# Kernel tuning notes

Measured on AMD Instinct MI355X. Metric: run time of the kernel, lower is better.

The kernel has to match this reference:

```python
import jax, jax.numpy as jnp
import numpy as np

BN_EPS = 1e-5


def setup_inputs() -> dict:
    key = jax.random.key(0)
    k1, k2 = jax.random.split(key, 2)
    b, C, h, w = 4, 256, 64, 64
    K = 16  # num_codes is hard-coded to 16 inside __init__
    x = jax.random.normal(k1, (b, C, h, w), dtype=jnp.float32)
    conv_w = jax.random.normal(k2, (K, C), dtype=jnp.float32) * (1.0 / np.sqrt(C))
    bn_gamma = jnp.ones((K,), dtype=jnp.float32)
    bn_beta = jnp.zeros((K,), dtype=jnp.float32)
    return {"x": x, "conv_w": conv_w, "bn_gamma": bn_gamma, "bn_beta": bn_beta}


def reference(x, conv_w, bn_gamma, bn_beta):
    b, C, h, w = x.shape
    K = conv_w.shape[0]
    hw = h * w

    # 1x1 conv (no bias) -> BatchNorm2d (training-mode batch stats) -> ReLU
    cw = jnp.einsum('kc,bchw->bkhw', conv_w, x)          # (b, K, h, w)
    mean = cw.mean(axis=(0, 2, 3))                        # (K,)
    var = cw.var(axis=(0, 2, 3))                          # biased variance, (K,)
    cw = (cw - mean[None, :, None, None]) * jax.lax.rsqrt(var + BN_EPS)[None, :, None, None]
    cw = cw * bn_gamma[None, :, None, None] + bn_beta[None, :, None, None]
    cw = jax.nn.relu(cw)

    cw_flat = cw.reshape(b, K, hw)                        # (b, K, hw)
    scale = cw_flat.mean(axis=2)                          # (b, K)
    # Faithful to torch: flat row-major reinterpretation of (b,K,hw) as (b,hw,K,1)
    r = cw_flat.reshape(b, hw, K, 1)                      # (b, hw, K, 1)

    x2 = x.reshape(b, C, hw).transpose(0, 2, 1)           # (b, hw, C)
    diff = x2[:, :, None, :] - r                          # (b, hw, K, C)

    scaled_l2 = scale[:, :, None] * jnp.sum(diff * diff, axis=1)   # (b, K, C)
    aw = jax.nn.softmax(scaled_l2, axis=1)                # softmax over K, (b, K, C)
    encoded_feat = jnp.sum(aw[:, None, :, :] * diff, axis=1)       # (b, K, C)
    return encoded_feat
```

## Files before the change

kernel.cpp:

```cpp
#include <hip/hip_runtime.h>

#define BN_EPS 1e-5f

#define OFF_PBN     0
#define OFF_PSR     16384
#define OFF_PSX     32768
#define OFF_PSXX    163840
#define OFF_CROSSR  294912
#define OFF_CW      360448
#define OFF_PCX     622592
#define WS_NEED     ((size_t)(OFF_PCX + 2097152) * sizeof(float))

#define FMA16(v, rp)                                     \
    {                                                    \
        const float4* rq_ = (const float4*)(rp);         \
        float4 r0_ = rq_[0], r1_ = rq_[1];               \
        float4 r2_ = rq_[2], r3_ = rq_[3];               \
        acc[0]  = fmaf(v, r0_.x, acc[0]);                \
        acc[1]  = fmaf(v, r0_.y, acc[1]);                \
        acc[2]  = fmaf(v, r0_.z, acc[2]);                \
        acc[3]  = fmaf(v, r0_.w, acc[3]);                \
        acc[4]  = fmaf(v, r1_.x, acc[4]);                \
        acc[5]  = fmaf(v, r1_.y, acc[5]);                \
        acc[6]  = fmaf(v, r1_.z, acc[6]);                \
        acc[7]  = fmaf(v, r1_.w, acc[7]);                \
        acc[8]  = fmaf(v, r2_.x, acc[8]);                \
        acc[9]  = fmaf(v, r2_.y, acc[9]);                \
        acc[10] = fmaf(v, r2_.z, acc[10]);               \
        acc[11] = fmaf(v, r2_.w, acc[11]);               \
        acc[12] = fmaf(v, r3_.x, acc[12]);               \
        acc[13] = fmaf(v, r3_.y, acc[13]);               \
        acc[14] = fmaf(v, r3_.z, acc[14]);               \
        acc[15] = fmaf(v, r3_.w, acc[15]);               \
    }

__global__ __launch_bounds__(256, 2) void k_conv(const float* __restrict__ x,
                                                 const float* __restrict__ wq,
                                                 float* __restrict__ cw,
                                                 float* __restrict__ pbn) {
    __shared__ float xl[10240];
    __shared__ float wlT[4124];
    __shared__ float comb[512];
    __shared__ float bnr1[128], bnr2[128];
    int bid = blockIdx.x;
    int b   = bid >> 7;
    int s   = bid & 127;
    int t   = threadIdx.x;
    int k   = t & 15;
    int q   = t >> 4;
    int iq  = q & 7;
    int h   = q >> 3;

    for (int m = t; m < 4096; m += 256) {
        int kk = m >> 8, c = m & 255;
        wlT[(c << 4) + ((c >> 5) << 2) + kk] = wq[m];
    }
    #pragma unroll
    for (int j = 0; j < 8; ++j) {
        int F  = j * 256 + t;
        int cc = F >> 3, i4 = F & 7;
        float4 v = *(const float4*)(x + (size_t)(b * 256 + cc) * 4096
                                    + s * 32 + i4 * 4);
        xl[cc * 40 + i4 * 4 + 0] = v.x;
        xl[cc * 40 + i4 * 4 + 1] = v.y;
        xl[cc * 40 + i4 * 4 + 2] = v.z;
        xl[cc * 40 + i4 * 4 + 3] = v.w;
    }
    __syncthreads();

    float a0 = 0.f, a1 = 0.f, a2 = 0.f, a3 = 0.f;
    int c0 = h * 128;
    #pragma unroll 8
    for (int cc = 0; cc < 128; ++cc) {
        int c = c0 + cc;
        float4 xv = *(const float4*)&xl[c * 40 + iq * 4];
        float wv  = wlT[(c << 4) + ((c >> 5) << 2) + k];
        a0 = fmaf(wv, xv.x, a0);
        a1 = fmaf(wv, xv.y, a1);
        a2 = fmaf(wv, xv.z, a2);
        a3 = fmaf(wv, xv.w, a3);
    }
    if (h == 1) {
        int p = t & 127;
        comb[p * 4 + 0] = a0; comb[p * 4 + 1] = a1;
        comb[p * 4 + 2] = a2; comb[p * 4 + 3] = a3;
    }
    __syncthreads();
    if (h == 0) {
        a0 += comb[t * 4 + 0]; a1 += comb[t * 4 + 1];
        a2 += comb[t * 4 + 2]; a3 += comb[t * 4 + 3];
        float4 o; o.x = a0; o.y = a1; o.z = a2; o.w = a3;
        *(float4*)(cw + (size_t)b * 65536 + (size_t)k * 4096 + s * 32 + iq * 4) = o;
        bnr1[iq * 16 + k] = a0 + a1 + a2 + a3;
        bnr2[iq * 16 + k] = a0 * a0 + a1 * a1 + a2 * a2 + a3 * a3;
    }
    __syncthreads();
    if (t < 16) {
        float s1 = 0.f, s2 = 0.f;
        #pragma unroll
        for (int j = 0; j < 8; ++j) { s1 += bnr1[j * 16 + t]; s2 += bnr2[j * 16 + t]; }
        pbn[bid * 32 + t]      = s1;
        pbn[bid * 32 + 16 + t] = s2;
    }
}

__global__ __launch_bounds__(256, 2) void k_main(const float* __restrict__ x,
                                                 const float* __restrict__ gamma,
                                                 const float* __restrict__ beta,
                                                 float* __restrict__ ws,
                                                 float* __restrict__ pcx) {
    __shared__ float xl[8192];
    __shared__ float rl[512];
    __shared__ float red1[256], red2[256];
    __shared__ float bnred[256];
    int bid = blockIdx.x;
    int b   = bid >> 7;
    int s   = bid & 127;
    int kp  = s >> 3;
    int t   = threadIdx.x;

    {
        int col = t & 31, row0 = t >> 5;
        float p = 0.f;
        for (int m = row0; m < 512; m += 8) p += ws[OFF_PBN + m * 32 + col];
        bnred[t] = p;
    }
    __syncthreads();
    float s1 = 0.f, s2 = 0.f;
    #pragma unroll
    for (int j = 0; j < 8; ++j) {
        s1 += bnred[j * 32 + kp];
        s2 += bnred[j * 32 + 16 + kp];
    }
    float mean = s1 * (1.f / 16384.f);
    float var  = s2 * (1.f / 16384.f) - mean * mean;
    float aa   = gamma[kp] * rsqrtf(var + BN_EPS);
    float bb   = beta[kp] - mean * aa;

    #pragma unroll
    for (int j = 0; j < 8; ++j) {
        int F  = j * 256 + t;
        int cc = F >> 3, i4 = F & 7;
        const float* pa = x + (size_t)(b * 256 + cc) * 4096 + s * 32 + i4 * 4;
        float4 v = *(const float4*)pa;
        int ib = i4 * 4;
        xl[(ib + 0) * 256 + (cc ^ (ib + 0))] = v.x;
        xl[(ib + 1) * 256 + (cc ^ (ib + 1))] = v.y;
        xl[(ib + 2) * 256 + (cc ^ (ib + 2))] = v.z;
        xl[(ib + 3) * 256 + (cc ^ (ib + 3))] = v.w;
    }

    const float* cwp = ws + OFF_CW + (size_t)b * 65536 + (size_t)kp * 4096
                     + (size_t)(s & 7) * 512;
    float sr = 0.f, srr = 0.f;
    #pragma unroll
    for (int j = 0; j < 2; ++j) {
        float v = cwp[t + j * 256];
        v = fmaxf(fmaf(v, aa, bb), 0.f);
        rl[t + j * 256] = v;
        sr += v; srr += v * v;
    }
    red1[t] = sr; red2[t] = srr;
    __syncthreads();

    if (t < 16) {
        float a1 = 0.f, a2 = 0.f;
        for (int m = t; m < 256; m += 16) { a1 += red1[m]; a2 += red2[m]; }
        ws[OFF_PSR + bid * 32 + t]      = a1;
        ws[OFF_PSR + bid * 32 + 16 + t] = a2;
    }

    int c = t;
    float acc[16];
    #pragma unroll
    for (int k = 0; k < 16; ++k) acc[k] = 0.f;
    float xs = 0.f, xs2 = 0.f;
    #pragma unroll
    for (int ii = 0; ii < 32; ++ii) {
        float xv = xl[ii * 256 + (c ^ ii)];
        xs += xv; xs2 += xv * xv;
        FMA16(xv, rl + ii * 16);
    }

    ws[OFF_PSX  + bid * 256 + c] = xs;
    ws[OFF_PSXX + bid * 256 + c] = xs2;
    float* pp = pcx + (size_t)(bid * 16) * 256 + c;
    #pragma unroll
    for (int k = 0; k < 16; ++k) pp[(size_t)k * 256] = acc[k];
}

__global__ __launch_bounds__(256) void k_red(const float* __restrict__ pcx,
                                             float* __restrict__ crossr) {
    int bid = blockIdx.x;
    int b  = bid >> 6;
    int k  = (bid >> 2) & 15;
    int sg = bid & 3;
    int c  = threadIdx.x;
    float acc = 0.f;
    #pragma unroll 8
    for (int m = 0; m < 32; ++m) {
        int sl = sg * 32 + m;
        acc += pcx[(size_t)((b * 128 + sl) * 16 + k) * 256 + c];
    }
    crossr[((sg * 4 + b) * 16 + k) * 256 + c] = acc;
}

__global__ __launch_bounds__(256) void k_final(const float* __restrict__ ws,
                                               float* __restrict__ out) {
    __shared__ float srl[4096];
    __shared__ float fin[48];
    int b = blockIdx.x;
    int t = threadIdx.x;

    const float* psr = ws + OFF_PSR + (size_t)b * 128 * 32;
    #pragma unroll
    for (int j = 0; j < 16; ++j) srl[j * 256 + t] = psr[j * 256 + t];
    __syncthreads();

    if (t < 16) {
        float v = 0.f;
        for (int s = 0; s < 128; ++s) v += srl[s * 32 + t];
        fin[t] = v;
    } else if (t < 32) {
        int k = t - 16;
        float v = 0.f;
        for (int s = 0; s < 128; ++s) v += srl[s * 32 + 16 + k];
        fin[16 + k] = v;
    } else if (t < 48) {
        int kp = t - 32;
        float v = 0.f;
        for (int s = kp * 8; s < kp * 8 + 8; ++s)
            for (int k2 = 0; k2 < 16; ++k2) v += srl[s * 32 + k2];
        fin[32 + kp] = v;
    }
    __syncthreads();

    int c = t;
    float sx = 0.f, sxx = 0.f;
    const float* psx  = ws + OFF_PSX  + (size_t)b * 128 * 256;
    const float* psxx = ws + OFF_PSXX + (size_t)b * 128 * 256;
    for (int p = 0; p < 128; ++p) {
        sx  += psx[p * 256 + c];
        sxx += psxx[p * 256 + c];
    }

    float sl2[16];
    float mx = -1e30f;
    #pragma unroll
    for (int k = 0; k < 16; ++k) {
        float cr = 0.f;
        #pragma unroll
        for (int sg = 0; sg < 4; ++sg)
            cr += ws[OFF_CROSSR + ((sg * 4 + b) * 16 + k) * 256 + c];
        float v = fin[32 + k] * (1.f / 4096.f) * (sxx - 2.f * cr + fin[16 + k]);
        sl2[k] = v;
        mx = fmaxf(mx, v);
    }
    float den = 0.f;
    #pragma unroll
    for (int k = 0; k < 16; ++k) {
        float e = __expf(sl2[k] - mx);
        sl2[k] = e;
        den += e;
    }
    float inv = 1.f / den;
    #pragma unroll
    for (int k = 0; k < 16; ++k)
        out[(size_t)(b * 16 + k) * 256 + c] = sl2[k] * inv * (sx - fin[k]);
}

extern "C" void kernel_launch(void* const* d_in, const int* in_sizes, int n_in,
                              void* d_out, int out_size, void* d_ws, size_t ws_size,
                              hipStream_t stream) {
    const float* x     = (const float*)d_in[0];
    const float* w     = (const float*)d_in[1];
    const float* gamma = (const float*)d_in[2];
    const float* beta  = (const float*)d_in[3];
    float* ws  = (float*)d_ws;
    float* out = (float*)d_out;

    k_conv<<<512, 256, 0, stream>>>(x, w, ws + OFF_CW, ws + OFF_PBN);
    k_main<<<512, 256, 0, stream>>>(x, gamma, beta, ws, ws + OFF_PCX);
    k_red<<<256, 256, 0, stream>>>(ws + OFF_PCX, ws + OFF_CROSSR);
    k_final<<<4, 256, 0, stream>>>(ws, out);
}
```

Measured before the change: 108.3 us.

## Move psx/psr partial reductions from 4-block final kernel into parallel reduce kernel

The serial reductions over 128 partial slices of psx, psxx and psr, previously done by only 4 blocks in k_final, now run in k_red. Its existing k=0/k=1 blocks reduce 32-slice chunks of psx/psxx, and 4 extra blocks reduce the psr stats into a small fin buffer. k_final then only sums 4 pre-reduced chunks and reads fin from global memory. The aim is to shorten the latency-bound tail in the 4-block kernel, at the cost of extra workspace traffic and some load imbalance in k_red. A few loop unroll pragmas are also added in k_main.

Result: faster. 89.42 us (-17.4%).

```diff
diff --git a/kernel.cpp b/kernel.cpp
--- a/kernel.cpp
+++ b/kernel.cpp
@@ -7,9 +7,10 @@
 #define OFF_PSX     32768
 #define OFF_PSXX    163840
 #define OFF_CROSSR  294912
-#define OFF_CW      360448
-#define OFF_PCX     622592
-#define WS_NEED     ((size_t)(OFF_PCX + 2097152) * sizeof(float))
+#define OFF_SXF     360448
+#define OFF_FIN     368640
+#define OFF_CW      368896
+#define OFF_PCX     631040
 
 #define FMA16(v, rp)                                     \
     {                                                    \
@@ -122,6 +123,7 @@
     {
         int col = t & 31, row0 = t >> 5;
         float p = 0.f;
+        #pragma unroll 16
         for (int m = row0; m < 512; m += 8) p += ws[OFF_PBN + m * 32 + col];
         bnred[t] = p;
     }
@@ -165,6 +167,7 @@
 
     if (t < 16) {
         float a1 = 0.f, a2 = 0.f;
+        #pragma unroll
         for (int m = t; m < 256; m += 16) { a1 += red1[m]; a2 += red2[m]; }
         ws[OFF_PSR + bid * 32 + t]      = a1;
         ws[OFF_PSR + bid * 32 + 16 + t] = a2;
@@ -190,58 +193,77 @@
 }
 
 __global__ __launch_bounds__(256) void k_red(const float* __restrict__ pcx,
-                                             float* __restrict__ crossr) {
+                                             float* __restrict__ ws) {
+    __shared__ float pred[16][32];
     int bid = blockIdx.x;
-    int b  = bid >> 6;
-    int k  = (bid >> 2) & 15;
-    int sg = bid & 3;
-    int c  = threadIdx.x;
-    float acc = 0.f;
-    #pragma unroll 8
-    for (int m = 0; m < 32; ++m) {
-        int sl = sg * 32 + m;
-        acc += pcx[(size_t)((b * 128 + sl) * 16 + k) * 256 + c];
-    }
-    crossr[((sg * 4 + b) * 16 + k) * 256 + c] = acc;
+    int t   = threadIdx.x;
+
+    if (bid < 256) {
+        int b  = bid >> 6;
+        int k  = (bid >> 2) & 15;
+        int sg = bid & 3;
+        int c  = t;
+        float acc = 0.f;
+        #pragma unroll
+        for (int m = 0; m < 32; ++m)
+            acc += pcx[(size_t)((b * 128 + sg * 32 + m) * 16 + k) * 256 + c];
+        ws[OFF_CROSSR + ((sg * 4 + b) * 16 + k) * 256 + c] = acc;
+
+        if (k == 0) {
+            float sv = 0.f;
+            #pragma unroll
+            for (int m = 0; m < 32; ++m)
+                sv += ws[OFF_PSX + (size_t)(b * 128 + sg * 32 + m) * 256 + c];
+            ws[OFF_SXF + ((b * 4 + sg) * 2 + 0) * 256 + c] = sv;
+        } else if (k == 1) {
+            float sv = 0.f;
+            #pragma unroll
+            for (int m = 0; m < 32; ++m)
+                sv += ws[OFF_PSXX + (size_t)(b * 128 + sg * 32 + m) * 256 + c];
+            ws[OFF_SXF + ((b * 4 + sg) * 2 + 1) * 256 + c] = sv;
+        }
+    } else {
+        int b   = bid - 256;
+        int col = t & 31, ch = t >> 5;
+        const float* psr = ws + OFF_PSR + (size_t)b * 128 * 32;
+        float p0 = 0.f, p1 = 0.f;
+        #pragma unroll
+        for (int j = 0; j < 8; ++j) p0 += psr[(ch * 16 + j) * 32 + col];
+        #pragma unroll
+        for (int j = 0; j < 8; ++j) p1 += psr[(ch * 16 + 8 + j) * 32 + col];
+        pred[ch * 2][col]     = p0;
+        pred[ch * 2 + 1][col] = p1;
+        __syncthreads();
+        if (t < 16) {
+            float v = 0.f;
+            #pragma unroll
+            for (int q2 = 0; q2 < 16; ++q2) v += pred[q2][t];
+            ws[OFF_FIN + b * 64 + t] = v;
+        } else if (t < 32) {
+            int k = t - 16;
+            float v = 0.f;
+            #pragma unroll
+            for (int q2 = 0; q2 < 16; ++q2) v += pred[q2][16 + k];
+            ws[OFF_FIN + b * 64 + 16 + k] = v;
+        } else if (t < 48) {
+            int kp = t - 32;
+            float v = 0.f;
+            #pragma unroll
+            for (int k2 = 0; k2 < 16; ++k2) v += pred[kp][k2];
+            ws[OFF_FIN + b * 64 + 32 + kp] = v;
+        }
+    }
 }
 
 __global__ __launch_bounds__(256) void k_final(const float* __restrict__ ws,
                                                float* __restrict__ out) {
-    __shared__ float srl[4096];
-    __shared__ float fin[48];
     int b = blockIdx.x;
-    int t = threadIdx.x;
-
-    const float* psr = ws + OFF_PSR + (size_t)b * 128 * 32;
-    #pragma unroll
-    for (int j = 0; j < 16; ++j) srl[j * 256 + t] = psr[j * 256 + t];
-    __syncthreads();
-
-    if (t < 16) {
-        float v = 0.f;
-        for (int s = 0; s < 128; ++s) v += srl[s * 32 + t];
-        fin[t] = v;
-    } else if (t < 32) {
-        int k = t - 16;
-        float v = 0.f;
-        for (int s = 0; s < 128; ++s) v += srl[s * 32 + 16 + k];
-        fin[16 + k] = v;
-    } else if (t < 48) {
-        int kp = t - 32;
-        float v = 0.f;
-        for (int s = kp * 8; s < kp * 8 + 8; ++s)
-            for (int k2 = 0; k2 < 16; ++k2) v += srl[s * 32 + k2];
-        fin[32 + kp] = v;
-    }
-    __syncthreads();
-
-    int c = t;
+    int c = threadIdx.x;
     float sx = 0.f, sxx = 0.f;
-    const float* psx  = ws + OFF_PSX  + (size_t)b * 128 * 256;
-    const float* psxx = ws + OFF_PSXX + (size_t)b * 128 * 256;
-    for (int p = 0; p < 128; ++p) {
-        sx  += psx[p * 256 + c];
-        sxx += psxx[p * 256 + c];
+    #pragma unroll
+    for (int sg = 0; sg < 4; ++sg) {
+        sx  += ws[OFF_SXF + ((b * 4 + sg) * 2 + 0) * 256 + c];
+        sxx += ws[OFF_SXF + ((b * 4 + sg) * 2 + 1) * 256 + c];
     }
 
     float sl2[16];
@@ -252,7 +274,8 @@
         #pragma unroll
         for (int sg = 0; sg < 4; ++sg)
             cr += ws[OFF_CROSSR + ((sg * 4 + b) * 16 + k) * 256 + c];
-        float v = fin[32 + k] * (1.f / 4096.f) * (sxx - 2.f * cr + fin[16 + k]);
+        float v = ws[OFF_FIN + b * 64 + 32 + k] * (1.f / 4096.f)
+                * (sxx - 2.f * cr + ws[OFF_FIN + b * 64 + 16 + k]);
         sl2[k] = v;
         mx = fmaxf(mx, v);
     }
@@ -266,7 +289,8 @@
     float inv = 1.f / den;
     #pragma unroll
     for (int k = 0; k < 16; ++k)
-        out[(size_t)(b * 16 + k) * 256 + c] = sl2[k] * inv * (sx - fin[k]);
+        out[(size_t)(b * 16 + k) * 256 + c]
+            = sl2[k] * inv * (sx - ws[OFF_FIN + b * 64 + k]);
 }
 
 extern "C" void kernel_launch(void* const* d_in, const int* in_sizes, int n_in,
@@ -281,6 +305,6 @@
 
     k_conv<<<512, 256, 0, stream>>>(x, w, ws + OFF_CW, ws + OFF_PBN);
     k_main<<<512, 256, 0, stream>>>(x, gamma, beta, ws, ws + OFF_PCX);
-    k_red<<<256, 256, 0, stream>>>(ws + OFF_PCX, ws + OFF_CROSSR);
+    k_red<<<260, 256, 0, stream>>>(ws + OFF_PCX, ws);
     k_final<<<4, 256, 0, stream>>>(ws, out);
 }
```
